# Performance work log

Measured on AMD Instinct MI355X. Metric: run time of the kernel, lower is better.

Reference implementation:

```python
import jax, jax.numpy as jnp
import numpy as np

KS = 3          # kernel size (forced by the view() shape constraint)
STRIDE = 1
PAD = 1
DIL = 1
K = KS * KS     # 9 taps


def _bilinear_sample(x, py, px):
    """x: [B,C,Hin,Win]; py,px: [B,C,K,H,W] float sample coords.
    Zero padding outside bounds (torchvision DeformConv semantics:
    each corner contributes only if it lies inside the image)."""
    B, C, Hin, Win = x.shape
    y0 = jnp.floor(py)
    x0 = jnp.floor(px)
    wy1 = py - y0
    wx1 = px - x0
    wy0 = 1.0 - wy1
    wx0 = 1.0 - wx1
    xf = x.reshape(B, C, Hin * Win)

    def gather(yi, xi):
        valid = (yi >= 0) & (yi <= Hin - 1) & (xi >= 0) & (xi <= Win - 1)
        yc = jnp.clip(yi, 0, Hin - 1).astype(jnp.int32)
        xc = jnp.clip(xi, 0, Win - 1).astype(jnp.int32)
        flat = (yc * Win + xc).reshape(B, C, -1)
        g = jnp.take_along_axis(xf, flat, axis=2).reshape(yi.shape)
        return jnp.where(valid, g, 0.0)

    return (wy0 * wx0 * gather(y0, x0)
            + wy0 * wx1 * gather(y0, x0 + 1)
            + wy1 * wx0 * gather(y0 + 1, x0)
            + wy1 * wx1 * gather(y0 + 1, x0 + 1))


def setup_inputs() -> dict:
    key = jax.random.key(0)
    ks = jax.random.split(key, 5)
    B, C, H, W = 8, 64, 128, 128
    Cout = 64
    return {
        "x": jax.random.normal(ks[0], (B, C, H, W), dtype=jnp.float32),
        # depthwise offset conv: groups=C, out = 18*C -> weight (18C, 1, 3, 3)
        "offset_w": jax.random.normal(ks[1], (2 * K * C, 1, 3, 3), dtype=jnp.float32) * 0.05,
        "offset_b": jax.random.normal(ks[2], (2 * K * C,), dtype=jnp.float32) * 0.05,
        "deform_w": jax.random.normal(ks[3], (Cout, C, KS, KS), dtype=jnp.float32) * 0.05,
        "deform_b": jax.random.normal(ks[4], (Cout,), dtype=jnp.float32) * 0.05,
    }


def reference(x, offset_w, offset_b, deform_w, deform_b):
    B, C, H, W = x.shape
    Cout = deform_w.shape[0]

    # 1) depthwise offset conv (groups = in_channels)
    off = jax.lax.conv_general_dilated(
        x, offset_w, window_strides=(STRIDE, STRIDE),
        padding=((PAD, PAD), (PAD, PAD)), rhs_dilation=(DIL, DIL),
        feature_group_count=C,
        dimension_numbers=("NCHW", "OIHW", "NCHW"))
    off = off + offset_b[None, :, None, None]

    # 2) softmax over the full channel axis (dim=1 in torch)
    off = jax.nn.softmax(off, axis=1)

    # 3) torchvision offset layout: channel 2*(g*K + k) + {0:dy, 1:dx},
    #    deformable_groups = C (per-input-channel offsets)
    off = off.reshape(B, C, K, 2, H, W)
    dy = off[:, :, :, 0]   # [B,C,K,H,W]
    dx = off[:, :, :, 1]

    base_y = (jnp.arange(H, dtype=x.dtype) * STRIDE - PAD)   # [H]
    base_x = (jnp.arange(W, dtype=x.dtype) * STRIDE - PAD)   # [W]
    ky = (jnp.repeat(jnp.arange(KS), KS) * DIL).astype(x.dtype)  # [K]
    kx = (jnp.tile(jnp.arange(KS), KS) * DIL).astype(x.dtype)

    py = base_y[None, None, None, :, None] + ky[None, None, :, None, None] + dy
    px = base_x[None, None, None, None, :] + kx[None, None, :, None, None] + dx

    sampled = _bilinear_sample(x, py, px)                    # [B,C,K,H,W]

    # 4) weighted accumulation over (c_in, kernel tap)
    out = jnp.einsum("bckhw,ock->bohw", sampled, deform_w.reshape(Cout, C, K))
    return out + deform_b[None, :, None, None]
```

## Files before the change

kernel.cpp:

```cpp
#include <hip/hip_runtime.h>

#define B_    8
#define C_    64
#define H_    128
#define W_    128
#define K_    9
#define J_    18
#define COUT_ 64
#define TPX   16
#define CK    576
#define SROW  584
#define NW81  (C_ * 81)
#define L2E   1.4426950408889634f

typedef __attribute__((ext_vector_type(8))) short short8;
typedef __attribute__((ext_vector_type(4))) float float4v;
typedef __attribute__((ext_vector_type(2))) float f32x2;

__device__ __forceinline__ unsigned short f2bf(float f) {
    unsigned int u = __float_as_uint(f);
    u = u + 0x7fffu + ((u >> 16) & 1u);
    return (unsigned short)(u >> 16);
}

constexpr int TMAP[9] = {0, 1, 2, 7, 8, 9, 14, 15, 16};

#define TRBLK (B_ * H_ * 2)
#define DWBLK ((CK * COUT_) / 256)
__global__ __launch_bounds__(256)
void pre_all(const float* __restrict__ x, float* __restrict__ xt,
             const float* __restrict__ dw, unsigned short* __restrict__ dwb,
             const float* __restrict__ ow, unsigned int* __restrict__ owp) {
    __shared__ float tile[64][65];
    const int bid = blockIdx.x;
    if (bid < TRBLK) {
        const int wt  = bid & 1;
        const int h   = (bid >> 1) & 127;
        const int b   = bid >> 8;
        const int w0  = wt << 6;
        const int q   = threadIdx.x >> 6;
        const int l   = threadIdx.x & 63;
        #pragma unroll
        for (int r = 0; r < 16; r++) {
            const int c = q * 16 + r;
            tile[c][l] = x[((size_t)(b * C_ + c) * H_ + h) * W_ + w0 + l];
        }
        __syncthreads();
        #pragma unroll
        for (int r = 0; r < 16; r++) {
            const int w = q * 16 + r;
            xt[((size_t)(b * H_ + h) * W_ + w0 + w) * C_ + l] = tile[l][w];
        }
    } else if (bid < TRBLK + DWBLK) {
        const int i = (bid - TRBLK) * 256 + threadIdx.x;
        dwb[i] = f2bf(dw[i]);
    } else {
        const int i = (bid - TRBLK - DWBLK) * 256 + threadIdx.x;
        if (i < NW81) {
            const int c = i / 81, r = i - c * 81;
            const int k = r / 9,  t = r - k * 9;
            const float* s = ow + c * 162 + k * 18 + t;
            owp[i] = (unsigned int)f2bf(s[0] * L2E) |
                     ((unsigned int)f2bf(s[9] * L2E) << 16);
        }
    }
}

__global__ __launch_bounds__(256)
void nchw_to_nhwc(const float* __restrict__ x, float* __restrict__ xt) {
    __shared__ float tile[64][65];
    const int bid = blockIdx.x;
    const int wt  = bid & 1;
    const int h   = (bid >> 1) & 127;
    const int b   = bid >> 8;
    const int w0  = wt << 6;
    const int q   = threadIdx.x >> 6;
    const int l   = threadIdx.x & 63;
    #pragma unroll
    for (int r = 0; r < 16; r++) {
        const int c = q * 16 + r;
        tile[c][l] = x[((size_t)(b * C_ + c) * H_ + h) * W_ + w0 + l];
    }
    __syncthreads();
    #pragma unroll
    for (int r = 0; r < 16; r++) {
        const int w = q * 16 + r;
        xt[((size_t)(b * H_ + h) * W_ + w0 + w) * C_ + l] = tile[l][w];
    }
}
__global__ __launch_bounds__(256)
void prep_dwb(const float* __restrict__ dw, unsigned short* __restrict__ dwb) {
    const int i = blockIdx.x * 256 + threadIdx.x;
    if (i < CK * COUT_) dwb[i] = f2bf(dw[i]);
}

template<int T>
__device__ __forceinline__ void conv_steps(const unsigned int* __restrict__ owc,
                                           const float (&S)[28], f32x2 (&v2)[4][9]) {
    if constexpr (T < 81) {
        const unsigned int pw = owc[T];
        const f32x2 w2 = {__uint_as_float(pw << 16),
                          __uint_as_float(pw & 0xffff0000u)};
        constexpr int k = T / 9;
        constexpr int p = TMAP[T % 9];
        #pragma unroll
        for (int px = 0; px < 4; px++) {
            const float s = S[p + px];
            v2[px][k] = __builtin_elementwise_fma(w2, (f32x2){s, s}, v2[px][k]);
        }
        conv_steps<T + 1>(owc, S, v2);
    }
}

template<int I>
__device__ __forceinline__ void taps_px(const f32x2 (&w)[9], const f32x2 inv2,
                                        const float (&S)[28],
                                        unsigned short* __restrict__ sb) {
    #pragma unroll
    for (int k = 0; k < 9; k++) {
        const f32x2 d2 = w[k] * inv2;
        const float dy = d2.x;
        const float dx = d2.y;
        const int base = TMAP[k] + I;
        const float a  = S[base],     bb = S[base + 1];
        const float c  = S[base + 7], dd = S[base + 8];
        const float top = fmaf(dx, bb - a, a);
        const float bot = fmaf(dx, dd - c, c);
        const float v   = fmaf(dy, bot - top, top);
        sb[k] = (unsigned short)(__float_as_uint(v) >> 16);
    }
}

template<bool NHWC>
__device__ __forceinline__ void load_strip(const float* __restrict__ xsrc,
                                           int b, int h, int wbase, int lane,
                                           float (&S)[28]) {
    if (h >= 1 && h <= H_ - 3 && wbase >= 1 && wbase <= W_ - 6) {
        const float* p0 = NHWC
            ? xsrc + ((size_t)(b * H_ + (h - 1)) * W_ + (wbase - 1)) * C_ + lane
            : xsrc + ((size_t)(b * C_ + lane) * H_ + (h - 1)) * W_ + (wbase - 1);
        const int rs = NHWC ? (W_ * C_) : W_;
        const int cs = NHWC ? C_ : 1;
        #pragma unroll
        for (int r = 0; r < 4; r++)
            #pragma unroll
            for (int s = 0; s < 7; s++)
                S[r * 7 + s] = p0[r * rs + s * cs];
    } else {
        #pragma unroll
        for (int r = 0; r < 4; r++) {
            const int y = h - 1 + r;
            const bool yv = (unsigned)y < (unsigned)H_;
            #pragma unroll
            for (int s = 0; s < 7; s++) {
                const int xx = wbase - 1 + s;
                const bool ok = yv && ((unsigned)xx < (unsigned)W_);
                const float* p = NHWC
                    ? xsrc + ((size_t)(b * H_ + (y & 127)) * W_ + (xx & 127)) * C_ + lane
                    : xsrc + ((size_t)(b * C_ + lane) * H_ + (y & 127)) * W_ + (xx & 127);
                S[r * 7 + s] = ok ? *p : 0.0f;
            }
        }
    }
}

__device__ __forceinline__ void phaseA(const unsigned int* __restrict__ owc,
                                       const float2* __restrict__ obp,
                                       const float (&S)[28],
                                       f32x2 (&v2)[4][9], float (&inv)[4]) {
    #pragma unroll
    for (int p = 0; p < 9; p++) {
        const float2 f = obp[p];
        const f32x2 b2 = {f.x * L2E, f.y * L2E};
        v2[0][p] = b2; v2[1][p] = b2; v2[2][p] = b2; v2[3][p] = b2;
    }
    conv_steps<0>(owc, S, v2);

    float psum[4];
    #pragma unroll
    for (int px = 0; px < 4; px++) {
        f32x2 ps2 = {0.0f, 0.0f};
        #pragma unroll
        for (int k = 0; k < 9; k++) {
            f32x2 e;
            e.x = __builtin_amdgcn_exp2f(v2[px][k].x);
            e.y = __builtin_amdgcn_exp2f(v2[px][k].y);
            v2[px][k] = e;
            ps2 += e;
        }
        psum[px] = ps2.x + ps2.y;
    }

    #pragma unroll
    for (int px = 0; px < 4; px++) psum[px] += __shfl_xor(psum[px], 32, 64);
#define RED_LEVEL(PAT) do { \
        const float r0_ = __uint_as_float((unsigned)__builtin_amdgcn_ds_swizzle((int)__float_as_uint(psum[0]), (PAT))); \
        const float r1_ = __uint_as_float((unsigned)__builtin_amdgcn_ds_swizzle((int)__float_as_uint(psum[1]), (PAT))); \
        const float r2_ = __uint_as_float((unsigned)__builtin_amdgcn_ds_swizzle((int)__float_as_uint(psum[2]), (PAT))); \
        const float r3_ = __uint_as_float((unsigned)__builtin_amdgcn_ds_swizzle((int)__float_as_uint(psum[3]), (PAT))); \
        psum[0] += r0_; psum[1] += r1_; psum[2] += r2_; psum[3] += r3_; \
    } while (0)
    RED_LEVEL(0x401F);
    RED_LEVEL(0x201F);
    RED_LEVEL(0x101F);
    RED_LEVEL(0x081F);
    RED_LEVEL(0x041F);
#undef RED_LEVEL

    inv[0] = __builtin_amdgcn_rcpf(psum[0]);
    inv[1] = __builtin_amdgcn_rcpf(psum[1]);
    inv[2] = __builtin_amdgcn_rcpf(psum[2]);
    inv[3] = __builtin_amdgcn_rcpf(psum[3]);
}

template<bool PREB>
__device__ __forceinline__ void phaseB(const unsigned short* __restrict__ arow,
                                       const unsigned short* __restrict__ bbase,
                                       const float* __restrict__ brow0,
                                       float bias, float* __restrict__ outp) {
    float4v acc = {0.f, 0.f, 0.f, 0.f};
    #pragma unroll
    for (int t = 0; t < 18; t++) {
        short8 afrag = *(const short8*)(arow + t * 32);
        short8 bfrag;
        if (PREB) {
            bfrag = *(const short8*)(bbase + t * 32);
        } else {
            const float* brow = brow0 + t * 32;
            float4 b0 = *(const float4*)brow;
            float4 b1 = *(const float4*)(brow + 4);
            union { short8 s8; unsigned short u[8]; } bfu;
            bfu.u[0] = f2bf(b0.x); bfu.u[1] = f2bf(b0.y); bfu.u[2] = f2bf(b0.z); bfu.u[3] = f2bf(b0.w);
            bfu.u[4] = f2bf(b1.x); bfu.u[5] = f2bf(b1.y); bfu.u[6] = f2bf(b1.z); bfu.u[7] = f2bf(b1.w);
            bfrag = bfu.s8;
        }
        acc = __builtin_amdgcn_mfma_f32_16x16x32_bf16(afrag, bfrag, acc, 0, 0, 0);
    }
    float4 res;
    res.x = acc[0] + bias; res.y = acc[1] + bias;
    res.z = acc[2] + bias; res.w = acc[3] + bias;
    *(float4*)outp = res;
}

template<bool NHWC, bool PREB, bool PREP>
__global__ __launch_bounds__(256, 3)
void dcn_fused(const float* __restrict__ xsrc,
               const float* __restrict__ ow,
               const unsigned int* __restrict__ owp,
               const float* __restrict__ ob,
               const float* __restrict__ dw,
               const unsigned short* __restrict__ dwb,
               const float* __restrict__ db,
               float* __restrict__ out) {
    __shared__ __align__(16) unsigned int ow_s[NW81];
    __shared__ __align__(16) unsigned short sbuf[TPX * SROW];

    const int tid  = threadIdx.x;
    const int wave = tid >> 6;
    const int lane = tid & 63;

    const int bid     = blockIdx.x;
    const int logical = (bid & 7) * 512 + (bid >> 3);
    const int b       = logical >> 9;
    const int rem     = logical & 511;
    const int h       = rem >> 2;
    const int w0base  = (rem & 3) << 5;

    if (PREP) {
        #pragma unroll
        for (int i = 0; i < 20; i++)
            ow_s[tid + i * 256] = owp[tid + i * 256];
        if (tid < 64) ow_s[5120 + tid] = owp[5120 + tid];
    } else {
        for (int i = tid; i < NW81; i += 256) {
            const int c = i / 81, r = i - c * 81;
            const int k = r / 9,  t = r - k * 9;
            const float* s = ow + c * 162 + k * 18 + t;
            ow_s[i] = (unsigned int)f2bf(s[0] * L2E) |
                      ((unsigned int)f2bf(s[9] * L2E) << 16);
        }
    }

    const int quad = lane >> 4;
    const int o    = (wave << 4) + (lane & 15);
    const unsigned int* owc = ow_s + lane * 81;
    const float2* obp = (const float2*)(ob + lane * J_);
    const unsigned short* arow  = sbuf + (lane & 15) * SROW + quad * 8;
    const unsigned short* bbase = PREB ? (dwb + (size_t)o * CK + quad * 8) : nullptr;
    const float* brow0 = PREB ? nullptr : (dw + (size_t)o * CK + quad * 8);
    const float bias = db[o];
    float* outrow = out + ((size_t)(b * COUT_ + o) * H_ + h) * W_ + w0base + (quad << 2);
    unsigned short* sb = sbuf + (wave << 2) * SROW + lane * K_;

    float S0[28];
    load_strip<NHWC>(xsrc, b, h, w0base + (wave << 2), lane, S0);

    __syncthreads();

    f32x2 v2a[4][9];
    float inva[4];
    phaseA(owc, obp, S0, v2a, inva);
    taps_px<0>(v2a[0], (f32x2){inva[0], inva[0]}, S0, sb);
    taps_px<1>(v2a[1], (f32x2){inva[1], inva[1]}, S0, sb + SROW);
    taps_px<2>(v2a[2], (f32x2){inva[2], inva[2]}, S0, sb + 2 * SROW);
    taps_px<3>(v2a[3], (f32x2){inva[3], inva[3]}, S0, sb + 3 * SROW);

    __syncthreads();

    float S1[28];
    load_strip<NHWC>(xsrc, b, h, w0base + 16 + (wave << 2), lane, S1);

    phaseB<PREB>(arow, bbase, brow0, bias, outrow);

    f32x2 v2b[4][9];
    float invb[4];
    phaseA(owc, obp, S1, v2b, invb);

    __syncthreads();

    taps_px<0>(v2b[0], (f32x2){invb[0], invb[0]}, S1, sb);
    taps_px<1>(v2b[1], (f32x2){invb[1], invb[1]}, S1, sb + SROW);
    taps_px<2>(v2b[2], (f32x2){invb[2], invb[2]}, S1, sb + 2 * SROW);
    taps_px<3>(v2b[3], (f32x2){invb[3], invb[3]}, S1, sb + 3 * SROW);

    __syncthreads();

    phaseB<PREB>(arow, bbase, brow0, bias, outrow + 16);
}

extern "C" void kernel_launch(void* const* d_in, const int* in_sizes, int n_in,
                              void* d_out, int out_size, void* d_ws, size_t ws_size,
                              hipStream_t stream) {
    (void)in_sizes; (void)n_in; (void)out_size;
    const float* x  = (const float*)d_in[0];
    const float* ow = (const float*)d_in[1];
    const float* ob = (const float*)d_in[2];
    const float* dw = (const float*)d_in[3];
    const float* db = (const float*)d_in[4];
    float* outp = (float*)d_out;

    const size_t xbytes  = (size_t)B_ * C_ * H_ * W_ * sizeof(float);
    const size_t dwbytes = (size_t)CK * COUT_ * sizeof(unsigned short);
    const size_t owbytes = (size_t)NW81 * sizeof(unsigned int);
    const dim3 grid(B_ * H_ * 4), blk(256);
    const int owblocks = (NW81 + 255) / 256;

    if (ws_size >= xbytes + dwbytes + owbytes) {
        float* xt = (float*)d_ws;
        unsigned short* dwb = (unsigned short*)((char*)d_ws + xbytes);
        unsigned int* owp = (unsigned int*)((char*)d_ws + xbytes + dwbytes);
        pre_all<<<dim3(TRBLK + DWBLK + owblocks), blk, 0, stream>>>(x, xt, dw, dwb, ow, owp);
        dcn_fused<true, true, true><<<grid, blk, 0, stream>>>(xt, ow, owp, ob, dw, dwb, db, outp);
    } else if (ws_size >= xbytes + dwbytes) {
        float* xt = (float*)d_ws;
        unsigned short* dwb = (unsigned short*)((char*)d_ws + xbytes);
        nchw_to_nhwc<<<dim3(B_ * H_ * 2), blk, 0, stream>>>(x, xt);
        prep_dwb<<<dim3((CK * COUT_ + 255) / 256), blk, 0, stream>>>(dw, dwb);
        dcn_fused<true, true, false><<<grid, blk, 0, stream>>>(xt, ow, nullptr, ob, dw, dwb, db, outp);
    } else if (ws_size >= xbytes) {
        float* xt = (float*)d_ws;
        nchw_to_nhwc<<<dim3(B_ * H_ * 2), blk, 0, stream>>>(x, xt);
        dcn_fused<true, false, false><<<grid, blk, 0, stream>>>(xt, ow, nullptr, ob, dw, nullptr, db, outp);
    } else {
        dcn_fused<false, false, false><<<grid, blk, 0, stream>>>(x, ow, nullptr, ob, dw, nullptr, db, outp);
    }
}
```

Before: 197.0 us.

## Double block size to 512 threads sharing offset weights, split MFMA accumulators

Each block now runs two independent groups of four waves, covering 64 output columns instead of 32. The per-block load of the offset-conv weights into shared memory is therefore amortized over twice the work, and the grid is halved. The phaseB MFMA chain is split into two accumulators to shorten the dependency chain. In exchange, shared memory per block roughly doubles and register pressure rises under launch_bounds(512,3), which may lower occupancy. The block-to-tile mapping also changes, dropping the previous batch-interleaved swizzle.

```diff
diff --git a/kernel.cpp b/kernel.cpp
--- a/kernel.cpp
+++ b/kernel.cpp
@@ -218,32 +218,39 @@
                                        const unsigned short* __restrict__ bbase,
                                        const float* __restrict__ brow0,
                                        float bias, float* __restrict__ outp) {
-    float4v acc = {0.f, 0.f, 0.f, 0.f};
-    #pragma unroll
-    for (int t = 0; t < 18; t++) {
-        short8 afrag = *(const short8*)(arow + t * 32);
-        short8 bfrag;
+    float4v acc0 = {0.f, 0.f, 0.f, 0.f};
+    float4v acc1 = {0.f, 0.f, 0.f, 0.f};
+    #pragma unroll
+    for (int t = 0; t < 18; t += 2) {
+        short8 af0 = *(const short8*)(arow + t * 32);
+        short8 af1 = *(const short8*)(arow + (t + 1) * 32);
+        short8 bf0, bf1;
         if (PREB) {
-            bfrag = *(const short8*)(bbase + t * 32);
+            bf0 = *(const short8*)(bbase + t * 32);
+            bf1 = *(const short8*)(bbase + (t + 1) * 32);
         } else {
-            const float* brow = brow0 + t * 32;
-            float4 b0 = *(const float4*)brow;
-            float4 b1 = *(const float4*)(brow + 4);
-            union { short8 s8; unsigned short u[8]; } bfu;
-            bfu.u[0] = f2bf(b0.x); bfu.u[1] = f2bf(b0.y); bfu.u[2] = f2bf(b0.z); bfu.u[3] = f2bf(b0.w);
-            bfu.u[4] = f2bf(b1.x); bfu.u[5] = f2bf(b1.y); bfu.u[6] = f2bf(b1.z); bfu.u[7] = f2bf(b1.w);
-            bfrag = bfu.s8;
-        }
-        acc = __builtin_amdgcn_mfma_f32_16x16x32_bf16(afrag, bfrag, acc, 0, 0, 0);
+            #pragma unroll
+            for (int u = 0; u < 2; u++) {
+                const float* brow = brow0 + (t + u) * 32;
+                float4 b0 = *(const float4*)brow;
+                float4 b1 = *(const float4*)(brow + 4);
+                union { short8 s8; unsigned short uu[8]; } bfu;
+                bfu.uu[0] = f2bf(b0.x); bfu.uu[1] = f2bf(b0.y); bfu.uu[2] = f2bf(b0.z); bfu.uu[3] = f2bf(b0.w);
+                bfu.uu[4] = f2bf(b1.x); bfu.uu[5] = f2bf(b1.y); bfu.uu[6] = f2bf(b1.z); bfu.uu[7] = f2bf(b1.w);
+                if (u == 0) bf0 = bfu.s8; else bf1 = bfu.s8;
+            }
+        }
+        acc0 = __builtin_amdgcn_mfma_f32_16x16x32_bf16(af0, bf0, acc0, 0, 0, 0);
+        acc1 = __builtin_amdgcn_mfma_f32_16x16x32_bf16(af1, bf1, acc1, 0, 0, 0);
     }
     float4 res;
-    res.x = acc[0] + bias; res.y = acc[1] + bias;
-    res.z = acc[2] + bias; res.w = acc[3] + bias;
+    res.x = (acc0[0] + acc1[0]) + bias; res.y = (acc0[1] + acc1[1]) + bias;
+    res.z = (acc0[2] + acc1[2]) + bias; res.w = (acc0[3] + acc1[3]) + bias;
     *(float4*)outp = res;
 }
 
 template<bool NHWC, bool PREB, bool PREP>
-__global__ __launch_bounds__(256, 3)
+__global__ __launch_bounds__(512, 3)
 void dcn_fused(const float* __restrict__ xsrc,
                const float* __restrict__ ow,
                const unsigned int* __restrict__ owp,
@@ -253,26 +260,27 @@
                const float* __restrict__ db,
                float* __restrict__ out) {
     __shared__ __align__(16) unsigned int ow_s[NW81];
-    __shared__ __align__(16) unsigned short sbuf[TPX * SROW];
+    __shared__ __align__(16) unsigned short sbuf[2 * TPX * SROW];
 
     const int tid  = threadIdx.x;
-    const int wave = tid >> 6;
+    const int w8   = tid >> 6;
     const int lane = tid & 63;
-
-    const int bid     = blockIdx.x;
-    const int logical = (bid & 7) * 512 + (bid >> 3);
-    const int b       = logical >> 9;
-    const int rem     = logical & 511;
-    const int h       = rem >> 2;
-    const int w0base  = (rem & 3) << 5;
+    const int grp  = w8 >> 2;
+    const int wl   = w8 & 3;
+
+    const int bid  = blockIdx.x;
+    const int b    = bid & 7;
+    const int rem  = bid >> 3;
+    const int h    = rem >> 1;
+    const int gbase = ((rem & 1) << 6) + (grp << 5);
 
     if (PREP) {
         #pragma unroll
-        for (int i = 0; i < 20; i++)
-            ow_s[tid + i * 256] = owp[tid + i * 256];
+        for (int i = 0; i < 10; i++)
+            ow_s[tid + i * 512] = owp[tid + i * 512];
         if (tid < 64) ow_s[5120 + tid] = owp[5120 + tid];
     } else {
-        for (int i = tid; i < NW81; i += 256) {
+        for (int i = tid; i < NW81; i += 512) {
             const int c = i / 81, r = i - c * 81;
             const int k = r / 9,  t = r - k * 9;
             const float* s = ow + c * 162 + k * 18 + t;
@@ -282,18 +290,19 @@
     }
 
     const int quad = lane >> 4;
-    const int o    = (wave << 4) + (lane & 15);
+    const int o    = (wl << 4) + (lane & 15);
     const unsigned int* owc = ow_s + lane * 81;
     const float2* obp = (const float2*)(ob + lane * J_);
-    const unsigned short* arow  = sbuf + (lane & 15) * SROW + quad * 8;
+    unsigned short* gsb = sbuf + grp * (TPX * SROW);
+    const unsigned short* arow  = gsb + (lane & 15) * SROW + quad * 8;
     const unsigned short* bbase = PREB ? (dwb + (size_t)o * CK + quad * 8) : nullptr;
     const float* brow0 = PREB ? nullptr : (dw + (size_t)o * CK + quad * 8);
     const float bias = db[o];
-    float* outrow = out + ((size_t)(b * COUT_ + o) * H_ + h) * W_ + w0base + (quad << 2);
-    unsigned short* sb = sbuf + (wave << 2) * SROW + lane * K_;
+    float* outrow = out + ((size_t)(b * COUT_ + o) * H_ + h) * W_ + gbase + (quad << 2);
+    unsigned short* sb = gsb + (wl << 2) * SROW + lane * K_;
 
     float S0[28];
-    load_strip<NHWC>(xsrc, b, h, w0base + (wave << 2), lane, S0);
+    load_strip<NHWC>(xsrc, b, h, gbase + (wl << 2), lane, S0);
 
     __syncthreads();
 
@@ -308,7 +317,7 @@
     __syncthreads();
 
     float S1[28];
-    load_strip<NHWC>(xsrc, b, h, w0base + 16 + (wave << 2), lane, S1);
+    load_strip<NHWC>(xsrc, b, h, gbase + 16 + (wl << 2), lane, S1);
 
     phaseB<PREB>(arow, bbase, brow0, bias, outrow);
 
@@ -342,26 +351,26 @@
     const size_t xbytes  = (size_t)B_ * C_ * H_ * W_ * sizeof(float);
     const size_t dwbytes = (size_t)CK * COUT_ * sizeof(unsigned short);
     const size_t owbytes = (size_t)NW81 * sizeof(unsigned int);
-    const dim3 grid(B_ * H_ * 4), blk(256);
+    const dim3 grid(B_ * H_ * 2), blk512(512), blk256(256);
     const int owblocks = (NW81 + 255) / 256;
 
     if (ws_size >= xbytes + dwbytes + owbytes) {
         float* xt = (float*)d_ws;
         unsigned short* dwb = (unsigned short*)((char*)d_ws + xbytes);
         unsigned int* owp = (unsigned int*)((char*)d_ws + xbytes + dwbytes);
-        pre_all<<<dim3(TRBLK + DWBLK + owblocks), blk, 0, stream>>>(x, xt, dw, dwb, ow, owp);
-        dcn_fused<true, true, true><<<grid, blk, 0, stream>>>(xt, ow, owp, ob, dw, dwb, db, outp);
+        pre_all<<<dim3(TRBLK + DWBLK + owblocks), blk256, 0, stream>>>(x, xt, dw, dwb, ow, owp);
+        dcn_fused<true, true, true><<<grid, blk512, 0, stream>>>(xt, ow, owp, ob, dw, dwb, db, outp);
     } else if (ws_size >= xbytes + dwbytes) {
         float* xt = (float*)d_ws;
         unsigned short* dwb = (unsigned short*)((char*)d_ws + xbytes);
-        nchw_to_nhwc<<<dim3(B_ * H_ * 2), blk, 0, stream>>>(x, xt);
-        prep_dwb<<<dim3((CK * COUT_ + 255) / 256), blk, 0, stream>>>(dw, dwb);
-        dcn_fused<true, true, false><<<grid, blk, 0, stream>>>(xt, ow, nullptr, ob, dw, dwb, db, outp);
+        nchw_to_nhwc<<<dim3(B_ * H_ * 2), blk256, 0, stream>>>(x, xt);
+        prep_dwb<<<dim3((CK * COUT_ + 255) / 256), blk256, 0, stream>>>(dw, dwb);
+        dcn_fused<true, true, false><<<grid, blk512, 0, stream>>>(xt, ow, nullptr, ob, dw, dwb, db, outp);
     } else if (ws_size >= xbytes) {
         float* xt = (float*)d_ws;
-        nchw_to_nhwc<<<dim3(B_ * H_ * 2), blk, 0, stream>>>(x, xt);
-        dcn_fused<true, false, false><<<grid, blk, 0, stream>>>(xt, ow, nullptr, ob, dw, nullptr, db, outp);
+        nchw_to_nhwc<<<dim3(B_ * H_ * 2), blk256, 0, stream>>>(x, xt);
+        dcn_fused<true, false, false><<<grid, blk512, 0, stream>>>(xt, ow, nullptr, ob, dw, nullptr, db, outp);
     } else {
-        dcn_fused<false, false, false><<<grid, blk, 0, stream>>>(x, ow, nullptr, ob, dw, nullptr, db, outp);
-    }
-}
+        dcn_fused<false, false, false><<<grid, blk512, 0, stream>>>(x, ow, nullptr, ob, dw, nullptr, db, outp);
+    }
+}
```

Result: slower. 234.7 us (+19.1%).
